# Optimization experiments

Hardware: AMD Instinct MI355X
Metric: run time of the kernel (lower is better)

Reference implementation:

```python
import jax, jax.numpy as jnp
import numpy as np


def positional_encoding(max_len, embed_dim):
    pos = jnp.arange(max_len, dtype=jnp.float32)[:, None]          # (L, 1)
    i = jnp.arange(embed_dim, dtype=jnp.float32)[None, :]          # (1, C)
    angle = pos / jnp.power(10000.0, 2.0 * jnp.floor(i / 2.0) / embed_dim)
    pe = jnp.where((jnp.arange(embed_dim) % 2) == 0, jnp.sin(angle), jnp.cos(angle))
    return pe[None, :, :]                                          # (1, L, C)


def setup_inputs() -> dict:
    key = jax.random.key(0)
    k1, k2 = jax.random.split(key)
    x = jax.random.normal(k1, (4, 256, 64, 64), dtype=jnp.float32)
    W_qkv = jax.random.normal(k2, (256, 768), dtype=jnp.float32) * 0.02
    return {"x": x, "W_qkv": W_qkv}


def reference(x, W_qkv):
    N, C, H, W = x.shape
    L = H * W
    num_heads = 8
    head_dim = C // num_heads

    # (N, C, H, W) -> (N, L, C), add sinusoidal positional encoding
    xt = x.reshape(N, C, L).transpose(0, 2, 1) + positional_encoding(L, C)

    # qkv projection (no bias): (N, L, 3C)
    qkv = xt @ W_qkv
    qkv = qkv.reshape(N, L, 3, num_heads, head_dim).transpose(2, 0, 3, 1, 4)
    q, k, v = qkv[0], qkv[1], qkv[2]                               # (N, h, L, d)

    scale = 1.0 / np.sqrt(head_dim).astype(np.float32)
    scores = jnp.einsum('nhqd,nhkd->nhqk', q, k) * scale           # (N, h, L, L)
    attn = jax.nn.softmax(scores, axis=-1)
    out = jnp.einsum('nhqk,nhkd->nhqd', attn, v)                   # (N, h, L, d)

    # (N, h, L, d) -> (N, L, C) -> (N, C, H, W)
    out = out.transpose(0, 2, 1, 3).reshape(N, L, C)
    return out.transpose(0, 2, 1).reshape(N, C, H, W)
```

## Files before the change

kernel.cpp:

```cpp
#include <hip/hip_runtime.h>
#include <hip/hip_bf16.h>

#define L_SEQ 4096
#define C_DIM 256
#define QKV_N 768

typedef short bf16x8 __attribute__((ext_vector_type(8)));
typedef float f32x4  __attribute__((ext_vector_type(4)));
typedef float f32x16 __attribute__((ext_vector_type(16)));

#if defined(__has_builtin)
#  if __has_builtin(__builtin_amdgcn_permlane32_swap)
#    define HAVE_PLSWAP 1
#  endif
#endif

__device__ inline short f2bf(float f){ union{__hip_bfloat16 h; short s;}u; u.h=__float2bfloat16(f); return u.s; }
__device__ inline float bf2f(short s){ union{unsigned u; float f;}x; x.u=((unsigned)(unsigned short)s)<<16; return x.f; }

__device__ inline unsigned cvtpk(float lo, float hi){
  unsigned r;
  asm("v_cvt_pk_bf16_f32 %0, %1, %2" : "=v"(r) : "v"(lo), "v"(hi));
  return r;
}

__device__ inline void plswap(unsigned &a, unsigned &b){
#ifdef HAVE_PLSWAP
  auto r = __builtin_amdgcn_permlane32_swap(a, b, false, false);
  a = r[0]; b = r[1];
#else
  unsigned ax = __shfl_xor((int)a, 32);
  unsigned bx = __shfl_xor((int)b, 32);
  bool hi = (threadIdx.x & 32) != 0;
  unsigned na = hi ? bx : a;
  unsigned nb = hi ? b : ax;
  a = na; b = nb;
#endif
}

__global__ __launch_bounds__(256) void tables_kernel(
    const float* __restrict__ W, short* __restrict__ pe_t, short* __restrict__ wT){
  int bid = blockIdx.x;
  if (bid < 4096){
    int idx = bid*256 + threadIdx.x;
    int c = idx >> 12, l = idx & 4095;
    int c2 = c & ~1;
    float inv = __expf(-(float)c2 * (9.210340371976184f/256.0f));
    float rev = (float)l * inv * 0.15915494309189535f;
    float fr = rev - floorf(rev);
    float v = (c & 1) ? __builtin_amdgcn_cosf(fr) : __builtin_amdgcn_sinf(fr);
    pe_t[idx] = f2bf(v);
  } else {
    int idx = (bid - 4096)*256 + threadIdx.x;
    int jj = idx >> 8, k = idx & 255;
    wT[idx] = f2bf(W[k*QKV_N + jj]);
  }
}

__global__ __launch_bounds__(256) void qkv_gemm(
    const float* __restrict__ x, const short* __restrict__ pe_t, const short* __restrict__ wT,
    short* __restrict__ qw, short* __restrict__ kw, short* __restrict__ vtw){
  __shared__ __align__(16) short A_lds[64][264];
  __shared__ __align__(16) short B_lds[2][192][40];
  int m0 = blockIdx.x * 64;
  int n = m0 >> 12, l0 = m0 & 4095;
  int j0 = blockIdx.y * 192;
  int tid = threadIdx.x;

  {
    int c = tid;
    const float* xp = x + ((size_t)n*C_DIM + c)*L_SEQ + l0;
    const short* pp = pe_t + (size_t)c*L_SEQ + l0;
    float xv[64];
#pragma unroll
    for (int q = 0; q < 16; ++q) *(float4*)&xv[q*4] = ((const float4*)xp)[q];
    short pv[64];
#pragma unroll
    for (int q = 0; q < 8; ++q) *(bf16x8*)&pv[q*8] = ((const bf16x8*)pp)[q];
#pragma unroll
    for (int i = 0; i < 64; ++i) A_lds[i][c] = f2bf(xv[i] + bf2f(pv[i]));
  }
  {
#pragma unroll
    for (int s = 0; s < 3; ++s){
      int chunk = tid + s*256;
      int j = chunk >> 2, kc = chunk & 3;
      *(bf16x8*)&B_lds[0][j][kc*8] = *(const bf16x8*)(wT + (size_t)(j0 + j)*256 + kc*8);
    }
  }
  __syncthreads();

  int wv = tid >> 6, lane = tid & 63, r = lane & 15, g = lane >> 4;
  f32x4 acc[4][3] = {};

  for (int ks = 0; ks < 8; ++ks){
    int buf = ks & 1;
    bf16x8 pre[3];
    if (ks < 7){
#pragma unroll
      for (int s = 0; s < 3; ++s){
        int chunk = tid + s*256;
        int j = chunk >> 2, kc = chunk & 3;
        pre[s] = *(const bf16x8*)(wT + (size_t)(j0 + j)*256 + (ks+1)*32 + kc*8);
      }
    }
    bf16x8 a[4];
#pragma unroll
    for (int mf = 0; mf < 4; ++mf)
      a[mf] = *(const bf16x8*)&A_lds[mf*16 + r][ks*32 + g*8];
#pragma unroll
    for (int t = 0; t < 3; ++t){
      bf16x8 b = *(const bf16x8*)&B_lds[buf][wv*48 + t*16 + r][g*8];
#pragma unroll
      for (int mf = 0; mf < 4; ++mf)
        acc[mf][t] = __builtin_amdgcn_mfma_f32_16x16x32_bf16(a[mf], b, acc[mf][t], 0,0,0);
    }
    if (ks < 7){
#pragma unroll
      for (int s = 0; s < 3; ++s){
        int chunk = tid + s*256;
        int j = chunk >> 2, kc = chunk & 3;
        *(bf16x8*)&B_lds[buf^1][j][kc*8] = pre[s];
      }
    }
    __syncthreads();
  }

  const float QSCALE = 0.17677669529663687f * 1.4426950408889634f;
#pragma unroll
  for (int mf = 0; mf < 4; ++mf)
#pragma unroll
  for (int t = 0; t < 3; ++t)
#pragma unroll
  for (int i = 0; i < 4; ++i){
    int l = l0 + mf*16 + g*4 + i;
    int j = j0 + wv*48 + t*16 + r;
    int which = j >> 8, h = (j >> 5) & 7, d = j & 31;
    int pair = n*8 + h;
    float v = acc[mf][t][i];
    if (which == 0)      qw[((size_t)pair*L_SEQ + l)*32 + d] = f2bf(v * QSCALE);
    else if (which == 1) kw[((size_t)pair*L_SEQ + l)*32 + d] = f2bf(v);
    else                 vtw[((size_t)pair*32 + d)*L_SEQ + l] = f2bf(v);
  }
}

__global__ __launch_bounds__(512,4) void attn_kernel(
    const short* __restrict__ qw, const short* __restrict__ kw,
    const short* __restrict__ vtw, float* __restrict__ out){
  __shared__ __align__(16) short K_lds[2][64][64];
  __shared__ __align__(16) short V_lds[2][32][64];
  const int KB = 64*64*2, VB = 32*64*2;

  int bid = blockIdx.x;
  int xcd = bid & 7, jj = bid >> 3;
  int pair = (jj >> 4)*8 + xcd;
  int q0 = (jj & 15)*256;
  int n = pair >> 3, h = pair & 7;
  int tid = threadIdx.x, wv = tid >> 6, lane = tid & 63;
  int qc = lane & 31, hi = lane >> 5;

  const short* qb_ = qw + (size_t)pair*L_SEQ*32;
  const short* kptr = kw + (size_t)pair*L_SEQ*32 + (size_t)(tid>>3)*32 + (tid&7)*4;
  const short* vptr = vtw + (size_t)pair*32*L_SEQ + (size_t)(tid>>4)*L_SEQ + (tid&15)*4;

  bf16x8 qf0 = *(const bf16x8*)(qb_ + (size_t)(q0 + wv*32 + qc)*32 + hi*8);
  bf16x8 qf1 = *(const bf16x8*)(qb_ + (size_t)(q0 + wv*32 + qc)*32 + 16 + hi*8);

  int skey = tid >> 3, sdc = tid & 7;
  int svd  = tid >> 4, svc = tid & 15;
  char* kdst = (char*)&K_lds[0][skey][0] + (((sdc>>1) ^ (skey&7))*16) + (sdc&1)*8;
  char* vdst = (char*)&V_lds[0][svd][0] + (((svc>>1) ^ (svd&7))*16) + (svc&1)*8;

  int ka_off[2][2];
#pragma unroll
  for (int sub = 0; sub < 2; ++sub)
#pragma unroll
  for (int dh = 0; dh < 2; ++dh){
    int row = sub*32 + qc;
    ka_off[sub][dh] = row*128 + (((dh*2 + hi) ^ (row & 7))*16);
  }
  int va_off[4];
#pragma unroll
  for (int m = 0; m < 4; ++m) va_off[m] = qc*128 + (((2*m + hi) ^ (qc & 7))*16);

  const bf16x8 onesv = {0x3F80,0x3F80,0x3F80,0x3F80,0x3F80,0x3F80,0x3F80,0x3F80};

  f32x16 o = {}, ls = {};

  {
    int2 kv = *(const int2*)kptr;
    int2 vv = *(const int2*)vptr;
    *(int2*)kdst = kv;
    *(int2*)vdst = vv;
  }
  __syncthreads();

  for (int t = 0; t < 64; ++t){
    int buf = t & 1;
    const char* kB_ = (const char*)K_lds + buf*KB;
    const char* vB_ = (const char*)V_lds + buf*VB;

    bf16x8 ka00 = *(const bf16x8*)(kB_ + ka_off[0][0]);
    bf16x8 ka01 = *(const bf16x8*)(kB_ + ka_off[0][1]);
    bf16x8 ka10 = *(const bf16x8*)(kB_ + ka_off[1][0]);
    bf16x8 ka11 = *(const bf16x8*)(kB_ + ka_off[1][1]);

    f32x16 z = {};
    __builtin_amdgcn_s_setprio(1);
    f32x16 s0 = __builtin_amdgcn_mfma_f32_32x32x16_bf16(ka00, qf0, z, 0,0,0);
    s0        = __builtin_amdgcn_mfma_f32_32x32x16_bf16(ka01, qf1, s0, 0,0,0);
    f32x16 s1 = __builtin_amdgcn_mfma_f32_32x32x16_bf16(ka10, qf0, z, 0,0,0);
    s1        = __builtin_amdgcn_mfma_f32_32x32x16_bf16(ka11, qf1, s1, 0,0,0);
    __builtin_amdgcn_s_setprio(0);

    int2 kv, vv;
    bool pf = (t < 63);
    if (pf){
      kptr += 64*32; vptr += 64;
      kv = *(const int2*)kptr;
      vv = *(const int2*)vptr;
    }

#pragma unroll
    for (int i = 0; i < 16; ++i) s0[i] = __builtin_amdgcn_exp2f(s0[i]);
#pragma unroll
    for (int i = 0; i < 16; ++i) s1[i] = __builtin_amdgcn_exp2f(s1[i]);

#pragma unroll
    for (int m = 0; m < 4; ++m){
      int b = (m & 1)*8;
      unsigned g0a, g0b, g4a, g4b;
      if (m < 2){
        g0a = cvtpk(s0[b+0], s0[b+1]); g0b = cvtpk(s0[b+2], s0[b+3]);
        g4a = cvtpk(s0[b+4], s0[b+5]); g4b = cvtpk(s0[b+6], s0[b+7]);
      } else {
        g0a = cvtpk(s1[b+0], s1[b+1]); g0b = cvtpk(s1[b+2], s1[b+3]);
        g4a = cvtpk(s1[b+4], s1[b+5]); g4b = cvtpk(s1[b+6], s1[b+7]);
      }
      plswap(g0a, g4a);
      plswap(g0b, g4b);
      union{ unsigned w[4]; bf16x8 v; } pu;
      pu.w[0] = g0a; pu.w[1] = g0b; pu.w[2] = g4a; pu.w[3] = g4b;
      bf16x8 va = *(const bf16x8*)(vB_ + va_off[m]);
      o  = __builtin_amdgcn_mfma_f32_32x32x16_bf16(va,    pu.v, o,  0,0,0);
      ls = __builtin_amdgcn_mfma_f32_32x32x16_bf16(onesv, pu.v, ls, 0,0,0);
    }

    if (pf){
      *(int2*)(kdst + (buf^1)*KB) = kv;
      *(int2*)(vdst + (buf^1)*VB) = vv;
    }
    __syncthreads();
  }

  float rinv = 1.0f / ls[0];
#pragma unroll
  for (int reg = 0; reg < 16; ++reg){
    int d = (reg & 3) + 8*(reg >> 2) + 4*hi;
    out[(size_t)(n*C_DIM + h*32 + d)*L_SEQ + q0 + wv*32 + qc] = o[reg]*rinv;
  }
}

extern "C" void kernel_launch(void* const* d_in, const int* in_sizes, int n_in,
                              void* d_out, int out_size, void* d_ws, size_t ws_size,
                              hipStream_t stream) {
  const float* x = (const float*)d_in[0];
  const float* W = (const float*)d_in[1];
  float* out = (float*)d_out;
  char* ws = (char*)d_ws;
  short* pe_t = (short*)ws;
  short* wT   = (short*)(ws + (size_t)2*1024*1024);
  short* qw   = (short*)(ws + (size_t)3*1024*1024);
  short* kw   = (short*)(ws + (size_t)11*1024*1024);
  short* vtw  = (short*)(ws + (size_t)19*1024*1024);

  tables_kernel<<<dim3(4864), 256, 0, stream>>>(W, pe_t, wT);
  qkv_gemm<<<dim3(256, 4), 256, 0, stream>>>(x, pe_t, wT, qw, kw, vtw);
  attn_kernel<<<dim3(512), 512, 0, stream>>>(qw, kw, vtw, out);
}
```

Before: 193.0 us.

## Software-pipeline PV MFMA of previous tile with exp of current tile

The attention loop is restructured so the P·V and row-sum MFMAs for tile t-1 run while the exp2 and bf16 packing of tile t's scores are computed. The packed probabilities are carried across iterations in registers, and the V double-buffer index is shifted by one tile. A zeroed V buffer handles the first iteration and an epilogue flushes the last tile. The goal is to hide the dependency between transcendental/VALU work and the matrix units. In exchange it adds an extra __syncthreads per iteration and more live registers, and the occupancy hint is lowered from 4 to 3.

Result: slower. 214.5 us (+11.1%).

```diff
diff --git a/kernel.cpp b/kernel.cpp
--- a/kernel.cpp
+++ b/kernel.cpp
@@ -144,7 +144,7 @@
   }
 }
 
-__global__ __launch_bounds__(512,4) void attn_kernel(
+__global__ __launch_bounds__(512,3) void attn_kernel(
     const short* __restrict__ qw, const short* __restrict__ kw,
     const short* __restrict__ vtw, float* __restrict__ out){
   __shared__ __align__(16) short K_lds[2][64][64];
@@ -186,24 +186,37 @@
   const bf16x8 onesv = {0x3F80,0x3F80,0x3F80,0x3F80,0x3F80,0x3F80,0x3F80,0x3F80};
 
   f32x16 o = {}, ls = {};
+  unsigned pu_prev[4][4];
+#pragma unroll
+  for (int m = 0; m < 4; ++m)
+#pragma unroll
+    for (int w = 0; w < 4; ++w) pu_prev[m][w] = 0u;
 
   {
     int2 kv = *(const int2*)kptr;
     int2 vv = *(const int2*)vptr;
     *(int2*)kdst = kv;
     *(int2*)vdst = vv;
+    if (tid < 256){
+      int4 zz = {0,0,0,0};
+      *(int4*)((char*)&V_lds[1][0][0] + tid*16) = zz;
+    }
   }
   __syncthreads();
 
   for (int t = 0; t < 64; ++t){
     int buf = t & 1;
     const char* kB_ = (const char*)K_lds + buf*KB;
-    const char* vB_ = (const char*)V_lds + buf*VB;
+    const char* vB_ = (const char*)V_lds + (buf^1)*VB;
 
     bf16x8 ka00 = *(const bf16x8*)(kB_ + ka_off[0][0]);
     bf16x8 ka01 = *(const bf16x8*)(kB_ + ka_off[0][1]);
     bf16x8 ka10 = *(const bf16x8*)(kB_ + ka_off[1][0]);
     bf16x8 ka11 = *(const bf16x8*)(kB_ + ka_off[1][1]);
+    bf16x8 va[4];
+#pragma unroll
+    for (int m = 0; m < 4; ++m) va[m] = *(const bf16x8*)(vB_ + va_off[m]);
+    __syncthreads();
 
     f32x16 z = {};
     __builtin_amdgcn_s_setprio(1);
@@ -222,10 +235,18 @@
     }
 
 #pragma unroll
+    for (int m = 0; m < 4; ++m){
+      union{ unsigned w[4]; bf16x8 v; } pu;
+      pu.w[0] = pu_prev[m][0]; pu.w[1] = pu_prev[m][1];
+      pu.w[2] = pu_prev[m][2]; pu.w[3] = pu_prev[m][3];
+      o  = __builtin_amdgcn_mfma_f32_32x32x16_bf16(va[m], pu.v, o,  0,0,0);
+      ls = __builtin_amdgcn_mfma_f32_32x32x16_bf16(onesv, pu.v, ls, 0,0,0);
+    }
+
+#pragma unroll
     for (int i = 0; i < 16; ++i) s0[i] = __builtin_amdgcn_exp2f(s0[i]);
 #pragma unroll
     for (int i = 0; i < 16; ++i) s1[i] = __builtin_amdgcn_exp2f(s1[i]);
-
 #pragma unroll
     for (int m = 0; m < 4; ++m){
       int b = (m & 1)*8;
@@ -239,11 +260,8 @@
       }
       plswap(g0a, g4a);
       plswap(g0b, g4b);
-      union{ unsigned w[4]; bf16x8 v; } pu;
-      pu.w[0] = g0a; pu.w[1] = g0b; pu.w[2] = g4a; pu.w[3] = g4b;
-      bf16x8 va = *(const bf16x8*)(vB_ + va_off[m]);
-      o  = __builtin_amdgcn_mfma_f32_32x32x16_bf16(va,    pu.v, o,  0,0,0);
-      ls = __builtin_amdgcn_mfma_f32_32x32x16_bf16(onesv, pu.v, ls, 0,0,0);
+      pu_prev[m][0] = g0a; pu_prev[m][1] = g0b;
+      pu_prev[m][2] = g4a; pu_prev[m][3] = g4b;
     }
 
     if (pf){
@@ -251,6 +269,21 @@
       *(int2*)(vdst + (buf^1)*VB) = vv;
     }
     __syncthreads();
+  }
+
+  {
+    const char* vB_ = (const char*)V_lds + 1*VB;
+    bf16x8 va[4];
+#pragma unroll
+    for (int m = 0; m < 4; ++m) va[m] = *(const bf16x8*)(vB_ + va_off[m]);
+#pragma unroll
+    for (int m = 0; m < 4; ++m){
+      union{ unsigned w[4]; bf16x8 v; } pu;
+      pu.w[0] = pu_prev[m][0]; pu.w[1] = pu_prev[m][1];
+      pu.w[2] = pu_prev[m][2]; pu.w[3] = pu_prev[m][3];
+      o  = __builtin_amdgcn_mfma_f32_32x32x16_bf16(va[m], pu.v, o,  0,0,0);
+      ls = __builtin_amdgcn_mfma_f32_32x32x16_bf16(onesv, pu.v, ls, 0,0,0);
+    }
   }
 
   float rinv = 1.0f / ls[0];
```
